# Kernel tuning notes

Measured on AMD Instinct MI355X. Metric: run time of the kernel, lower is better.

Reference implementation:

```python
import jax, jax.numpy as jnp
import numpy as np

CHEB_K = 3
HIDDEN = 64
HORIZON = 12
OUT_DIM = 1


def _supports(E, K):
    # adaptive adjacency: softmax(relu(E E^T)) rows, Chebyshev polynomial stack [K, N, N]
    A = jax.nn.softmax(jax.nn.relu(E @ E.T), axis=1)
    N = E.shape[0]
    s = [jnp.eye(N, dtype=E.dtype), A]
    for _ in range(2, K):
        s.append(2.0 * (A @ s[-1]) - s[-2])
    return jnp.stack(s, axis=0)


def _gconv(x, supports, W, b):
    # x: [B,N,C], supports: [K,N,N], W: [N,K,C,O], b: [N,O] -> [B,N,O]
    xg = jnp.einsum('knm,bmc->bnkc', supports, x)
    return jnp.einsum('bnkc,nkco->bno', xg, W) + b


def _agcrn_layer(x_seq, supports, gW, gb, uW, ub):
    # x_seq: [B,T,N,C]; returns full hidden sequence [B,T,N,H]
    B, T, N, _ = x_seq.shape
    h0 = jnp.zeros((B, N, HIDDEN), dtype=x_seq.dtype)

    def step(h, x):
        zr = jax.nn.sigmoid(_gconv(jnp.concatenate([x, h], axis=-1), supports, gW, gb))
        z, r = zr[..., :HIDDEN], zr[..., HIDDEN:]
        hc = jnp.tanh(_gconv(jnp.concatenate([x, z * h], axis=-1), supports, uW, ub))
        h_new = r * h + (1.0 - r) * hc
        return h_new, h_new

    _, hs = jax.lax.scan(step, h0, jnp.swapaxes(x_seq, 0, 1))  # [T,B,N,H]
    return jnp.swapaxes(hs, 0, 1)


def _forward(source, E, pools, conv_w, conv_b):
    supports = _supports(E, CHEB_K)
    cur = source
    for (gwp, gbp, uwp, ubp) in pools:
        # per-node weights from embedding pool (hoisted: E is constant over time)
        gW = jnp.einsum('nd,dkio->nkio', E, gwp)
        gb = E @ gbp
        uW = jnp.einsum('nd,dkio->nkio', E, uwp)
        ub = E @ ubp
        cur = _agcrn_layer(cur, supports, gW, gb, uW, ub)
    last = cur[:, -1]  # [B,N,H]
    # end_conv: Conv2d(1, horizon*out_dim, kernel=(1,H)) == linear over H per node
    y = jnp.einsum('bnh,oh->bon', last, conv_w) + conv_b[None, :, None]  # [B, horizon*out, N]
    B, _, N = y.shape
    y = y.reshape(B, HORIZON, OUT_DIM, N).transpose(0, 1, 3, 2)  # [B, horizon, N, out_dim]
    return y


def setup_inputs() -> dict:
    key = jax.random.key(0)
    ks = jax.random.split(key, 12)
    B, T, N, C, D, H = 64, 12, 2000, 1, 16, HIDDEN
    s = 0.1  # keep gates/tanh unsaturated
    return {
        'source': jax.random.normal(ks[0], (B, T, N, C), jnp.float32),
        'node_embeddings': jax.random.normal(ks[1], (N, D), jnp.float32),
        'gate_wpool_0': jax.random.normal(ks[2], (D, CHEB_K, C + H, 2 * H), jnp.float32) * s,
        'gate_bpool_0': jax.random.normal(ks[3], (D, 2 * H), jnp.float32) * s,
        'update_wpool_0': jax.random.normal(ks[4], (D, CHEB_K, C + H, H), jnp.float32) * s,
        'update_bpool_0': jax.random.normal(ks[5], (D, H), jnp.float32) * s,
        'gate_wpool_1': jax.random.normal(ks[6], (D, CHEB_K, 2 * H, 2 * H), jnp.float32) * s,
        'gate_bpool_1': jax.random.normal(ks[7], (D, 2 * H), jnp.float32) * s,
        'update_wpool_1': jax.random.normal(ks[8], (D, CHEB_K, 2 * H, H), jnp.float32) * s,
        'update_bpool_1': jax.random.normal(ks[9], (D, H), jnp.float32) * s,
        'conv_w': jax.random.normal(ks[10], (HORIZON * OUT_DIM, H), jnp.float32) * s,
        'conv_b': jax.random.normal(ks[11], (HORIZON * OUT_DIM,), jnp.float32) * s,
    }


def reference(source, node_embeddings, gate_wpool_0, gate_bpool_0, update_wpool_0,
              update_bpool_0, gate_wpool_1, gate_bpool_1, update_wpool_1,
              update_bpool_1, conv_w, conv_b):
    pools = [
        (gate_wpool_0, gate_bpool_0, update_wpool_0, update_bpool_0),
        (gate_wpool_1, gate_bpool_1, update_wpool_1, update_bpool_1),
    ]
    return _forward(source, node_embeddings, pools, conv_w, conv_b)
```

## Files before the change

### kernel.cpp

```cpp
#include <hip/hip_runtime.h>
#include <hip/hip_bf16.h>
#include <math.h>

#define NN 2000
#define DD 16
#define BB 64
#define TT 12
#define HH 64
#define MR 4000
#define SCL 2048.0f
#define ISCL (1.0f / 2048.0f)

typedef _Float16 f16;
typedef __attribute__((ext_vector_type(8))) _Float16 frag8h;
typedef __attribute__((ext_vector_type(4))) float floatx4;

__device__ inline float fin(float v) {
  return (v == v && v > -1e30f && v < 1e30f) ? v : 0.f;
}
__device__ inline float sigmoid_safe(float x) {
  float e = expf(-fabsf(x));
  float s = 1.f / (1.f + e);
  return x >= 0.f ? s : 1.f - s;
}
__device__ inline float tanh_safe(float x) {
  float e = expf(-2.f * fabsf(x));
  float r = (1.f - e) / (1.f + e);
  return x >= 0.f ? r : -r;
}
__device__ inline void split16(float v, f16& hi, f16& lo) {
  hi = (f16)v;
  lo = (f16)((v - (float)hi) * SCL);
}
__device__ inline void gll16(const void* g, void* l) {
  __builtin_amdgcn_global_load_lds((const __attribute__((address_space(1))) void*)g,
                                   (__attribute__((address_space(3))) void*)l, 16, 0, 0);
}

__global__ void kzero(float* p, int n) {
  int i = blockIdx.x * 256 + threadIdx.x;
  if (i < n) p[i] = 0.f;
}

__global__ __launch_bounds__(256) void ka(const float* __restrict__ E,
                                          float* __restrict__ A) {
  __shared__ float s[NN];
  __shared__ float red[256];
  int n = blockIdx.x;
  float en[DD];
#pragma unroll
  for (int d = 0; d < DD; ++d) en[d] = fin(E[n * DD + d]);
  float lmax = 0.f;
  for (int m = threadIdx.x; m < NN; m += 256) {
    float acc = 0.f;
#pragma unroll
    for (int d = 0; d < DD; ++d) acc += en[d] * fin(E[m * DD + d]);
    acc = fmaxf(acc, 0.f);
    s[m] = acc;
    lmax = fmaxf(lmax, acc);
  }
  red[threadIdx.x] = lmax;
  __syncthreads();
  for (int w = 128; w > 0; w >>= 1) {
    if (threadIdx.x < w) red[threadIdx.x] = fmaxf(red[threadIdx.x], red[threadIdx.x + w]);
    __syncthreads();
  }
  float mx = red[0];
  __syncthreads();
  float lsum = 0.f;
  for (int m = threadIdx.x; m < NN; m += 256) {
    float e = expf(s[m] - mx);
    s[m] = e;
    lsum += e;
  }
  red[threadIdx.x] = lsum;
  __syncthreads();
  for (int w = 128; w > 0; w >>= 1) {
    if (threadIdx.x < w) red[threadIdx.x] += red[threadIdx.x + w];
    __syncthreads();
  }
  float inv = 1.f / red[0];
  for (int m = threadIdx.x; m < NN; m += 256) A[(size_t)n * NN + m] = s[m] * inv;
}

#define TM 64
#define TK 32
__global__ __launch_bounds__(256) void kg(const float* __restrict__ A,
                                          const float* __restrict__ V,
                                          float* __restrict__ C, int cols) {
  __shared__ float As[TK][TM + 1];
  __shared__ float Bs[TK][TM + 1];
  int r0 = blockIdx.x * TM;
  int c0 = blockIdx.y * TM;
  int tid = threadIdx.x;
  int tx = tid % 16;
  int ty = tid / 16;
  float acc[4][4];
#pragma unroll
  for (int i = 0; i < 4; ++i)
#pragma unroll
    for (int j = 0; j < 4; ++j) acc[i][j] = 0.f;
  for (int k0 = 0; k0 < NN; k0 += TK) {
    for (int i = tid; i < TM * TK; i += 256) {
      int rr = i / TK, kk = i % TK;
      int gr = r0 + rr, gk = k0 + kk;
      As[kk][rr] = (gr < NN && gk < NN) ? A[(size_t)gr * NN + gk] : 0.f;
    }
    for (int i = tid; i < TK * TM; i += 256) {
      int kk = i / TM, cc = i % TM;
      int gk = k0 + kk, gc = c0 + cc;
      Bs[kk][cc] = (gk < NN && gc < cols) ? V[(size_t)gk * cols + gc] : 0.f;
    }
    __syncthreads();
#pragma unroll 4
    for (int kk = 0; kk < TK; ++kk) {
      float a[4], b[4];
#pragma unroll
      for (int i = 0; i < 4; ++i) a[i] = As[kk][ty * 4 + i];
#pragma unroll
      for (int j = 0; j < 4; ++j) b[j] = Bs[kk][tx * 4 + j];
#pragma unroll
      for (int i = 0; i < 4; ++i)
#pragma unroll
        for (int j = 0; j < 4; ++j) acc[i][j] += a[i] * b[j];
    }
    __syncthreads();
  }
#pragma unroll
  for (int i = 0; i < 4; ++i) {
    int gr = r0 + ty * 4 + i;
    if (gr >= NN) continue;
#pragma unroll
    for (int j = 0; j < 4; ++j) {
      int gc = c0 + tx * 4 + j;
      if (gc < cols) C[(size_t)gr * cols + gc] = acc[i][j];
    }
  }
}

__global__ void ksplitM(const float* __restrict__ A, const float* __restrict__ A2,
                        f16* __restrict__ Mh, f16* __restrict__ Ml) {
  int i = blockIdx.x * 256 + threadIdx.x;
  if (i >= MR * NN) return;
  int m = i / NN;
  int k = i % NN;
  float v;
  if (m < NN) v = A[(size_t)m * NN + k];
  else {
    int mm = m - NN;
    v = 2.f * A2[(size_t)mm * NN + k] - (mm == k ? 1.f : 0.f);
  }
  f16 hi, lo;
  split16(v, hi, lo);
  Mh[i] = hi;
  Ml[i] = lo;
}

__global__ __launch_bounds__(256) void kconvT(const float* __restrict__ V,
                                              f16* __restrict__ Th,
                                              f16* __restrict__ Tl, int cols) {
  __shared__ float sh[32][33];
  int k0 = blockIdx.x * 32;
  int c0 = blockIdx.y * 32;
  int tx = threadIdx.x % 32;
  int ty = threadIdx.x / 32;
#pragma unroll
  for (int i = 0; i < 4; ++i) {
    int r = k0 + ty + i * 8;
    int c = c0 + tx;
    sh[ty + i * 8][tx] = (r < NN && c < cols) ? V[(size_t)r * cols + c] : 0.f;
  }
  __syncthreads();
#pragma unroll
  for (int i = 0; i < 4; ++i) {
    int cc = c0 + ty + i * 8;
    int kk = k0 + tx;
    if (cc < cols && kk < NN) {
      f16 hi, lo;
      split16(sh[tx][ty + i * 8], hi, lo);
      Th[(size_t)cc * NN + kk] = hi;
      Tl[(size_t)cc * NN + kk] = lo;
    }
  }
}

#define KT 32
__global__ __launch_bounds__(256, 2) void kmm(const f16* __restrict__ Mh,
                                              const f16* __restrict__ Ml,
                                              const f16* __restrict__ Bh,
                                              const f16* __restrict__ Bl,
                                              float* __restrict__ C1,
                                              float* __restrict__ C2, int cols) {
  __shared__ __align__(16) f16 Ash[128 * KT];
  __shared__ __align__(16) f16 Asl[128 * KT];
  __shared__ __align__(16) f16 Bsh[128 * KT];
  __shared__ __align__(16) f16 Bsl[128 * KT];
  int tid = threadIdx.x;
  int lane = tid & 63;
  int wave = tid >> 6;
  int wr = wave >> 1;
  int wc = wave & 1;
  int bx = blockIdx.x;
  int by = blockIdx.y;
  floatx4 acc0[4][4], acc1[4][4];
#pragma unroll
  for (int i = 0; i < 4; ++i)
#pragma unroll
    for (int j = 0; j < 4; ++j) {
      acc0[i][j] = (floatx4){0.f, 0.f, 0.f, 0.f};
      acc1[i][j] = (floatx4){0.f, 0.f, 0.f, 0.f};
    }
  const frag8h zf = {0, 0, 0, 0, 0, 0, 0, 0};

  auto comp = [&]() {
    frag8h ah[4], al[4], bh[4], bl[4];
#pragma unroll
    for (int mi = 0; mi < 4; ++mi) {
      int jr = wr * 4 + mi;
      ah[mi] = *(const frag8h*)(&Ash[jr * 512 + lane * 8]);
      al[mi] = *(const frag8h*)(&Asl[jr * 512 + lane * 8]);
    }
#pragma unroll
    for (int ni = 0; ni < 4; ++ni) {
      int jc = wc * 4 + ni;
      bh[ni] = *(const frag8h*)(&Bsh[jc * 512 + lane * 8]);
      bl[ni] = *(const frag8h*)(&Bsl[jc * 512 + lane * 8]);
    }
#pragma unroll
    for (int mi = 0; mi < 4; ++mi)
#pragma unroll
      for (int ni = 0; ni < 4; ++ni) {
        acc0[mi][ni] = __builtin_amdgcn_mfma_f32_16x16x32_f16(ah[mi], bh[ni], acc0[mi][ni], 0, 0, 0);
        acc1[mi][ni] = __builtin_amdgcn_mfma_f32_16x16x32_f16(ah[mi], bl[ni], acc1[mi][ni], 0, 0, 0);
        acc1[mi][ni] = __builtin_amdgcn_mfma_f32_16x16x32_f16(al[mi], bh[ni], acc1[mi][ni], 0, 0, 0);
      }
  };

  const int lr = lane & 15;
  const int lq = lane >> 4;
  for (int k0 = 0; k0 + KT <= NN; k0 += KT) {
#pragma unroll
    for (int jj = 0; jj < 2; ++jj) {
      int j = wave * 2 + jj;
      int r = j * 16 + lr;
      size_t ko = (size_t)k0 + lq * 8;
      int gra = bx * 128 + r;
      if (gra < MR) {
        gll16(Mh + (size_t)gra * NN + ko, Ash + j * 512);
        gll16(Ml + (size_t)gra * NN + ko, Asl + j * 512);
      }
      int grb = by * 128 + r;
      if (grb < cols) {
        gll16(Bh + (size_t)grb * NN + ko, Bsh + j * 512);
        gll16(Bl + (size_t)grb * NN + ko, Bsl + j * 512);
      }
    }
    __syncthreads();
    comp();
    __syncthreads();
  }
  {
    int k0 = (NN / KT) * KT;
    if (k0 < NN) {
      for (int c = tid; c < 512; c += 256) {
        int j = c >> 6;
        int ll = c & 63;
        int q = ll >> 4;
        int rr = ll & 15;
        int r = j * 16 + rr;
        int gk = k0 + q * 8;
        bool kok = (gk + 8 <= NN);
        int gra = bx * 128 + r;
        bool aok = kok && (gra < MR);
        size_t ga = (size_t)gra * NN + gk;
        *(frag8h*)(&Ash[c * 8]) = aok ? *(const frag8h*)(Mh + ga) : zf;
        *(frag8h*)(&Asl[c * 8]) = aok ? *(const frag8h*)(Ml + ga) : zf;
        int grb = by * 128 + r;
        bool bok = kok && (grb < cols);
        size_t gb = (size_t)grb * NN + gk;
        *(frag8h*)(&Bsh[c * 8]) = bok ? *(const frag8h*)(Bh + gb) : zf;
        *(frag8h*)(&Bsl[c * 8]) = bok ? *(const frag8h*)(Bl + gb) : zf;
      }
      __syncthreads();
      comp();
      __syncthreads();
    }
  }
#pragma unroll
  for (int mi = 0; mi < 4; ++mi) {
#pragma unroll
    for (int ni = 0; ni < 4; ++ni) {
#pragma unroll
      for (int reg = 0; reg < 4; ++reg) {
        int row = bx * 128 + wr * 64 + mi * 16 + (lane >> 4) * 4 + reg;
        int col = by * 128 + wc * 64 + ni * 16 + (lane & 15);
        if (col >= cols || row >= MR) continue;
        float v = acc0[mi][ni][reg] + acc1[mi][ni][reg] * ISCL;
        if (row < NN) C1[(size_t)row * cols + col] = v;
        else C2[(size_t)(row - NN) * cols + col] = v;
      }
    }
  }
}

__global__ void kx(const float* __restrict__ src, float* __restrict__ xb,
                   int t, int b0, int CB) {
  int i = blockIdx.x * 256 + threadIdx.x;
  if (i >= NN * CB) return;
  int bb = i % CB;
  int n = i / CB;
  xb[i] = fin(src[((size_t)(b0 + bb) * TT + t) * NN + n]);
}

__global__ void kmulz(float* __restrict__ zb, const float* __restrict__ h, int n) {
  int i = blockIdx.x * 256 + threadIdx.x;
  if (i < n) zb[i] = zb[i] * h[i];
}

template <int O, int CB>
__global__ __launch_bounds__(256) void kgc(
    const float* __restrict__ x0, const float* __restrict__ x1, const float* __restrict__ x2,
    const float* __restrict__ wp, int Ctot, int base_c, int nC,
    const float* __restrict__ E, const float* __restrict__ bp,
    int act, int accum, float* outA, float* outB,
    int update, const float* __restrict__ rb, float* hio) {
  __shared__ float xs[8][CB + 1];
  __shared__ float ws[8][O];
  __shared__ float esm[DD];
  int n = blockIdx.x;
  int tid = threadIdx.x;
  int to = tid % 16;
  int tb = tid / 16;
  if (tid < DD) esm[tid] = fin(E[n * DD + tid]);
  __syncthreads();
  constexpr int NO = O / 16;
  constexpr int NB = CB / 16;
  float acc[NB][NO];
#pragma unroll
  for (int i = 0; i < NB; ++i)
#pragma unroll
    for (int j = 0; j < NO; ++j) acc[i][j] = 0.f;
  const size_t nb = (size_t)n * CB;
  for (int k = 0; k < 3; ++k) {
    const float* xk = (k == 0) ? x0 : (k == 1) ? x1 : x2;
    for (int c0 = 0; c0 < nC; c0 += 8) {
      int chunk = (nC - c0 < 8) ? (nC - c0) : 8;
      for (int i = tid; i < chunk * CB; i += 256) {
        int cc = i % chunk;
        int b = i / chunk;
        xs[cc][b] = xk[(nb + b) * nC + c0 + cc];
      }
      for (int i = tid; i < chunk * O; i += 256) {
        int o = i % O;
        int cc = i / O;
        int crow = base_c + c0 + cc;
        float wa = 0.f;
#pragma unroll
        for (int d = 0; d < DD; ++d)
          wa += esm[d] * fin(wp[((size_t)(d * 3 + k) * Ctot + crow) * O + o]);
        ws[cc][o] = wa;
      }
      __syncthreads();
      for (int cc = 0; cc < chunk; ++cc) {
        float xv[NB];
#pragma unroll
        for (int i = 0; i < NB; ++i) xv[i] = xs[cc][tb + 16 * i];
#pragma unroll
        for (int j = 0; j < NO; ++j) {
          float wv = ws[cc][to + 16 * j];
#pragma unroll
          for (int i = 0; i < NB; ++i) acc[i][j] += xv[i] * wv;
        }
      }
      __syncthreads();
    }
  }
#pragma unroll
  for (int i2 = 0; i2 < NB; ++i2) {
    int b = tb + 16 * i2;
#pragma unroll
    for (int j = 0; j < NO; ++j) {
      int o = to + 16 * j;
      float r = acc[i2][j];
      float* dst = (o < HH || !outB) ? (outA + (nb + b) * HH + (o % HH))
                                     : (outB + (nb + b) * HH + (o - HH));
      if (accum) r += *dst;
      if (bp) {
        float ba = 0.f;
#pragma unroll
        for (int d = 0; d < DD; ++d) ba += esm[d] * fin(bp[d * O + o]);
        r += ba;
      }
      r = fin(r);
      if (act == 1) r = sigmoid_safe(r);
      else if (act == 2) r = tanh_safe(r);
      if (update) {
        float rg = rb[(nb + b) * HH + o];
        float hold = hio[(nb + b) * HH + o];
        hio[(nb + b) * HH + o] = rg * hold + (1.f - rg) * r;
      } else {
        *dst = r;
      }
    }
  }
}

__global__ void kfin(const float* __restrict__ h1, const float* __restrict__ cw,
                     const float* __restrict__ cb, float* __restrict__ out,
                     int b0, int CB) {
  int idx = blockIdx.x * 256 + threadIdx.x;
  if (idx >= CB * TT * NN) return;
  int n = idx % NN;
  int o = (idx / NN) % TT;
  int bb = idx / (NN * TT);
  const float* hp = h1 + ((size_t)n * CB + bb) * HH;
  float acc = fin(cb[o]);
#pragma unroll
  for (int hh = 0; hh < HH; ++hh) acc += hp[hh] * fin(cw[o * HH + hh]);
  out[((size_t)(b0 + bb) * TT + o) * NN + n] = fin(acc);
}

template <int CB>
static void run_chunks(const float* src, const float* E,
                       const float* gwp0, const float* gbp0,
                       const float* uwp0, const float* ubp0,
                       const float* gwp1, const float* gbp1,
                       const float* uwp1, const float* ubp1,
                       const float* cw, const float* cb,
                       float* out, f16* Mh, f16* Ml,
                       char* wsp, size_t off0, hipStream_t stream) {
  size_t off = off0;
  auto allocf = [&](size_t nelem) {
    float* p = (float*)(wsp + off);
    off += (nelem * 4 + 255) & ~(size_t)255;
    return p;
  };
  auto alloch = [&](size_t nelem) {
    f16* p = (f16*)(wsp + off);
    off += (nelem * 2 + 255) & ~(size_t)255;
    return p;
  };
  const int C = CB * HH;
  const size_t NC = (size_t)NN * C;
  float* P1  = allocf(NC);
  float* P2  = allocf(NC);
  float* h0  = allocf(NC);
  float* h1  = allocf(NC);
  float* zb  = allocf(NC);
  float* rbf = allocf(NC);
  float* hc  = allocf(NC);
  f16* vh = alloch(NC);
  f16* vl = alloch(NC);
  float* xb0 = allocf((size_t)NN * CB);
  float* xb1 = allocf((size_t)NN * CB);
  float* xb2 = allocf((size_t)NN * CB);
  f16* xth = alloch((size_t)NN * CB);
  f16* xtl = alloch((size_t)NN * CB);

  const int EW = (int)((NC + 255) / 256);
  const int EWS = (NN * CB + 255) / 256;
  const dim3 gConv((NN + 31) / 32, (C + 31) / 32);
  const dim3 gConvX((NN + 31) / 32, (CB + 31) / 32);
  const dim3 gMM((MR + 127) / 128, (C + 127) / 128);
  const dim3 gMMX((MR + 127) / 128, (CB + 127) / 128);
  float* nul = nullptr;

  auto chain = [&](const float* V) {
    kconvT<<<gConv, 256, 0, stream>>>(V, vh, vl, C);
    kmm<<<gMM, 256, 0, stream>>>(Mh, Ml, vh, vl, P1, P2, C);
  };

  for (int b0 = 0; b0 < BB; b0 += CB) {
    kzero<<<EW, 256, 0, stream>>>(h0, (int)NC);
    kzero<<<EW, 256, 0, stream>>>(h1, (int)NC);
    for (int t = 0; t < TT; ++t) {
      kx<<<EWS, 256, 0, stream>>>(src, xb0, t, b0, CB);
      kconvT<<<gConvX, 256, 0, stream>>>(xb0, xth, xtl, CB);
      kmm<<<gMMX, 256, 0, stream>>>(Mh, Ml, xth, xtl, xb1, xb2, CB);
      chain(h0);
      kgc<128, CB><<<NN, 256, 0, stream>>>(h0, P1, P2, gwp0, 65, 1, 64, E, nullptr,
                                           0, 0, zb, rbf, 0, nul, nul);
      kgc<128, CB><<<NN, 256, 0, stream>>>(xb0, xb1, xb2, gwp0, 65, 0, 1, E, gbp0,
                                           1, 1, zb, rbf, 0, nul, nul);
      kgc<64, CB><<<NN, 256, 0, stream>>>(xb0, xb1, xb2, uwp0, 65, 0, 1, E, nullptr,
                                          0, 0, hc, nul, 0, nul, nul);
      kmulz<<<EW, 256, 0, stream>>>(zb, h0, (int)NC);
      chain(zb);
      kgc<64, CB><<<NN, 256, 0, stream>>>(zb, P1, P2, uwp0, 65, 1, 64, E, ubp0,
                                          2, 1, hc, nul, 1, rbf, h0);
      chain(h1);
      kgc<128, CB><<<NN, 256, 0, stream>>>(h1, P1, P2, gwp1, 128, 64, 64, E, nullptr,
                                           0, 0, zb, rbf, 0, nul, nul);
      chain(h0);
      kgc<128, CB><<<NN, 256, 0, stream>>>(h0, P1, P2, gwp1, 128, 0, 64, E, gbp1,
                                           1, 1, zb, rbf, 0, nul, nul);
      kgc<64, CB><<<NN, 256, 0, stream>>>(h0, P1, P2, uwp1, 128, 0, 64, E, nullptr,
                                          0, 0, hc, nul, 0, nul, nul);
      kmulz<<<EW, 256, 0, stream>>>(zb, h1, (int)NC);
      chain(zb);
      kgc<64, CB><<<NN, 256, 0, stream>>>(zb, P1, P2, uwp1, 128, 64, 64, E, ubp1,
                                          2, 1, hc, nul, 1, rbf, h1);
    }
    kfin<<<(CB * TT * NN + 255) / 256, 256, 0, stream>>>(h1, cw, cb, out, b0, CB);
  }
}

extern "C" void kernel_launch(void* const* d_in, const int* in_sizes, int n_in,
                              void* d_out, int out_size, void* d_ws, size_t ws_size,
                              hipStream_t stream) {
  const float* src  = (const float*)d_in[0];
  const float* E    = (const float*)d_in[1];
  const float* gwp0 = (const float*)d_in[2];
  const float* gbp0 = (const float*)d_in[3];
  const float* uwp0 = (const float*)d_in[4];
  const float* ubp0 = (const float*)d_in[5];
  const float* gwp1 = (const float*)d_in[6];
  const float* gbp1 = (const float*)d_in[7];
  const float* uwp1 = (const float*)d_in[8];
  const float* ubp1 = (const float*)d_in[9];
  const float* cw   = (const float*)d_in[10];
  const float* cb   = (const float*)d_in[11];
  float* out = (float*)d_out;
  (void)in_sizes; (void)n_in; (void)out_size;

  char* wsp = (char*)d_ws;
  size_t off = 0;
  f16* Mh = (f16*)(wsp + off); off += ((size_t)MR * NN * 2 + 255) & ~(size_t)255;
  f16* Ml = (f16*)(wsp + off); off += ((size_t)MR * NN * 2 + 255) & ~(size_t)255;
  size_t off0 = off;
  float* A  = (float*)(wsp + off0);
  float* A2 = (float*)(wsp + off0 + (((size_t)NN * NN * 4 + 255) & ~(size_t)255));

  ka<<<NN, 256, 0, stream>>>(E, A);
  {
    dim3 g((NN + TM - 1) / TM, (NN + TM - 1) / TM);
    kg<<<g, 256, 0, stream>>>(A, A, A2, NN);
  }
  ksplitM<<<(MR * NN + 255) / 256, 256, 0, stream>>>(A, A2, Mh, Ml);

  if (ws_size >= (size_t)320 * 1000 * 1000) {
    run_chunks<64>(src, E, gwp0, gbp0, uwp0, ubp0, gwp1, gbp1, uwp1, ubp1,
                   cw, cb, out, Mh, Ml, wsp, off0, stream);
  } else if (ws_size >= (size_t)185 * 1000 * 1000) {
    run_chunks<32>(src, E, gwp0, gbp0, uwp0, ubp0, gwp1, gbp1, uwp1, ubp1,
                   cw, cb, out, Mh, Ml, wsp, off0, stream);
  } else {
    run_chunks<16>(src, E, gwp0, gbp0, uwp0, ubp0, gwp1, gbp1, uwp1, ubp1,
                   cw, cb, out, Mh, Ml, wsp, off0, stream);
  }
}
```

Before: 61.85 ms.

## Batch input graph propagation over time, skip t=0 chains, reuse h0 propagation, swizzle XCDs

```diff
diff --git a/kernel.cpp b/kernel.cpp
--- a/kernel.cpp
+++ b/kernel.cpp
@@ -200,8 +200,14 @@
   int wave = tid >> 6;
   int wr = wave >> 1;
   int wc = wave & 1;
-  int bx = blockIdx.x;
-  int by = blockIdx.y;
+  int gx = gridDim.x;
+  int nwg = gx * gridDim.y;
+  int wg = blockIdx.y * gx + blockIdx.x;
+  int q = nwg >> 3, r = nwg & 7;
+  int xcd = wg & 7, lid = wg >> 3;
+  int swz = (xcd < r ? xcd * (q + 1) : r * (q + 1) + (xcd - r) * q) + lid;
+  int bx = swz % gx;
+  int by = swz / gx;
   floatx4 acc0[4][4], acc1[4][4];
 #pragma unroll
   for (int i = 0; i < 4; ++i)
@@ -242,14 +248,14 @@
 #pragma unroll
     for (int jj = 0; jj < 2; ++jj) {
       int j = wave * 2 + jj;
-      int r = j * 16 + lr;
+      int r2 = j * 16 + lr;
       size_t ko = (size_t)k0 + lq * 8;
-      int gra = bx * 128 + r;
+      int gra = bx * 128 + r2;
       if (gra < MR) {
         gll16(Mh + (size_t)gra * NN + ko, Ash + j * 512);
         gll16(Ml + (size_t)gra * NN + ko, Asl + j * 512);
       }
-      int grb = by * 128 + r;
+      int grb = by * 128 + r2;
       if (grb < cols) {
         gll16(Bh + (size_t)grb * NN + ko, Bsh + j * 512);
         gll16(Bl + (size_t)grb * NN + ko, Bsl + j * 512);
@@ -265,17 +271,17 @@
       for (int c = tid; c < 512; c += 256) {
         int j = c >> 6;
         int ll = c & 63;
-        int q = ll >> 4;
+        int qq = ll >> 4;
         int rr = ll & 15;
-        int r = j * 16 + rr;
-        int gk = k0 + q * 8;
+        int r2 = j * 16 + rr;
+        int gk = k0 + qq * 8;
         bool kok = (gk + 8 <= NN);
-        int gra = bx * 128 + r;
+        int gra = bx * 128 + r2;
         bool aok = kok && (gra < MR);
         size_t ga = (size_t)gra * NN + gk;
         *(frag8h*)(&Ash[c * 8]) = aok ? *(const frag8h*)(Mh + ga) : zf;
         *(frag8h*)(&Asl[c * 8]) = aok ? *(const frag8h*)(Ml + ga) : zf;
-        int grb = by * 128 + r;
+        int grb = by * 128 + r2;
         bool bok = kok && (grb < cols);
         size_t gb = (size_t)grb * NN + gk;
         *(frag8h*)(&Bsh[c * 8]) = bok ? *(const frag8h*)(Bh + gb) : zf;
@@ -312,6 +318,16 @@
   xb[i] = fin(src[((size_t)(b0 + bb) * TT + t) * NN + n]);
 }
 
+__global__ void kxa(const float* __restrict__ src, float* __restrict__ xa,
+                    int b0, int CB) {
+  int i = blockIdx.x * 256 + threadIdx.x;
+  if (i >= NN * TT * CB) return;
+  int bb = i % CB;
+  int t = (i / CB) % TT;
+  int n = i / (CB * TT);
+  xa[i] = fin(src[((size_t)(b0 + bb) * TT + t) * NN + n]);
+}
+
 __global__ void kmulz(float* __restrict__ zb, const float* __restrict__ h, int n) {
   int i = blockIdx.x * 256 + threadIdx.x;
   if (i < n) zb[i] = zb[i] * h[i];
@@ -320,7 +336,7 @@
 template <int O, int CB>
 __global__ __launch_bounds__(256) void kgc(
     const float* __restrict__ x0, const float* __restrict__ x1, const float* __restrict__ x2,
-    const float* __restrict__ wp, int Ctot, int base_c, int nC,
+    const float* __restrict__ wp, int Ctot, int base_c, int nC, int ldn,
     const float* __restrict__ E, const float* __restrict__ bp,
     int act, int accum, float* outA, float* outB,
     int update, const float* __restrict__ rb, float* hio) {
@@ -341,6 +357,7 @@
 #pragma unroll
     for (int j = 0; j < NO; ++j) acc[i][j] = 0.f;
   const size_t nb = (size_t)n * CB;
+  const size_t nx = (size_t)n * ldn;
   for (int k = 0; k < 3; ++k) {
     const float* xk = (k == 0) ? x0 : (k == 1) ? x1 : x2;
     for (int c0 = 0; c0 < nC; c0 += 8) {
@@ -348,7 +365,7 @@
       for (int i = tid; i < chunk * CB; i += 256) {
         int cc = i % chunk;
         int b = i / chunk;
-        xs[cc][b] = xk[(nb + b) * nC + c0 + cc];
+        xs[cc][b] = xk[nx + (size_t)b * nC + c0 + cc];
       }
       for (int i = tid; i < chunk * O; i += 256) {
         int o = i % O;
@@ -428,7 +445,7 @@
                        const float* uwp1, const float* ubp1,
                        const float* cw, const float* cb,
                        float* out, f16* Mh, f16* Ml,
-                       char* wsp, size_t off0, hipStream_t stream) {
+                       char* wsp, size_t off0, bool roomy, hipStream_t stream) {
   size_t off = off0;
   auto allocf = [&](size_t nelem) {
     float* p = (float*)(wsp + off);
@@ -441,6 +458,7 @@
     return p;
   };
   const int C = CB * HH;
+  const int XC = TT * CB;
   const size_t NC = (size_t)NN * C;
   float* P1  = allocf(NC);
   float* P2  = allocf(NC);
@@ -451,55 +469,107 @@
   float* hc  = allocf(NC);
   f16* vh = alloch(NC);
   f16* vl = alloch(NC);
-  float* xb0 = allocf((size_t)NN * CB);
-  float* xb1 = allocf((size_t)NN * CB);
-  float* xb2 = allocf((size_t)NN * CB);
-  f16* xth = alloch((size_t)NN * CB);
-  f16* xtl = alloch((size_t)NN * CB);
+  float *P1c = nullptr, *P2c = nullptr;
+  float *xa = nullptr, *xb1a = nullptr, *xb2a = nullptr;
+  float *xb0 = nullptr, *xb1 = nullptr, *xb2 = nullptr;
+  f16 *xth, *xtl;
+  if (roomy) {
+    P1c = allocf(NC);
+    P2c = allocf(NC);
+    xa   = allocf((size_t)NN * XC);
+    xb1a = allocf((size_t)NN * XC);
+    xb2a = allocf((size_t)NN * XC);
+    xth = alloch((size_t)NN * XC);
+    xtl = alloch((size_t)NN * XC);
+  } else {
+    xb0 = allocf((size_t)NN * CB);
+    xb1 = allocf((size_t)NN * CB);
+    xb2 = allocf((size_t)NN * CB);
+    xth = alloch((size_t)NN * CB);
+    xtl = alloch((size_t)NN * CB);
+  }
 
   const int EW = (int)((NC + 255) / 256);
-  const int EWS = (NN * CB + 255) / 256;
   const dim3 gConv((NN + 31) / 32, (C + 31) / 32);
-  const dim3 gConvX((NN + 31) / 32, (CB + 31) / 32);
   const dim3 gMM((MR + 127) / 128, (C + 127) / 128);
-  const dim3 gMMX((MR + 127) / 128, (CB + 127) / 128);
   float* nul = nullptr;
 
-  auto chain = [&](const float* V) {
+  auto chain_to = [&](const float* V, float* D1, float* D2) {
     kconvT<<<gConv, 256, 0, stream>>>(V, vh, vl, C);
-    kmm<<<gMM, 256, 0, stream>>>(Mh, Ml, vh, vl, P1, P2, C);
+    kmm<<<gMM, 256, 0, stream>>>(Mh, Ml, vh, vl, D1, D2, C);
   };
 
   for (int b0 = 0; b0 < BB; b0 += CB) {
     kzero<<<EW, 256, 0, stream>>>(h0, (int)NC);
     kzero<<<EW, 256, 0, stream>>>(h1, (int)NC);
+    if (roomy) {
+      kxa<<<((NN * XC) + 255) / 256, 256, 0, stream>>>(src, xa, b0, CB);
+      dim3 gcx((NN + 31) / 32, (XC + 31) / 32);
+      kconvT<<<gcx, 256, 0, stream>>>(xa, xth, xtl, XC);
+      dim3 gmx((MR + 127) / 128, (XC + 127) / 128);
+      kmm<<<gmx, 256, 0, stream>>>(Mh, Ml, xth, xtl, xb1a, xb2a, XC);
+    }
     for (int t = 0; t < TT; ++t) {
-      kx<<<EWS, 256, 0, stream>>>(src, xb0, t, b0, CB);
-      kconvT<<<gConvX, 256, 0, stream>>>(xb0, xth, xtl, CB);
-      kmm<<<gMMX, 256, 0, stream>>>(Mh, Ml, xth, xtl, xb1, xb2, CB);
-      chain(h0);
-      kgc<128, CB><<<NN, 256, 0, stream>>>(h0, P1, P2, gwp0, 65, 1, 64, E, nullptr,
+      const bool tz = (t == 0);
+      const float *xt0, *xt1, *xt2;
+      int xln;
+      if (roomy) {
+        xt0 = xa + t * CB;
+        xt1 = xb1a + t * CB;
+        xt2 = xb2a + t * CB;
+        xln = XC;
+      } else {
+        kx<<<(NN * CB + 255) / 256, 256, 0, stream>>>(src, xb0, t, b0, CB);
+        dim3 gcx((NN + 31) / 32, (CB + 31) / 32);
+        kconvT<<<gcx, 256, 0, stream>>>(xb0, xth, xtl, CB);
+        dim3 gmx((MR + 127) / 128, (CB + 127) / 128);
+        kmm<<<gmx, 256, 0, stream>>>(Mh, Ml, xth, xtl, xb1, xb2, CB);
+        xt0 = xb0; xt1 = xb1; xt2 = xb2;
+        xln = CB;
+      }
+      const float *g1, *g2;
+      if (tz) { g1 = h0; g2 = h0; }
+      else if (roomy) { g1 = P1c; g2 = P2c; }
+      else { chain_to(h0, P1, P2); g1 = P1; g2 = P2; }
+      kgc<128, CB><<<NN, 256, 0, stream>>>(h0, g1, g2, gwp0, 65, 1, 64, C, E, nullptr,
                                            0, 0, zb, rbf, 0, nul, nul);
-      kgc<128, CB><<<NN, 256, 0, stream>>>(xb0, xb1, xb2, gwp0, 65, 0, 1, E, gbp0,
+      kgc<128, CB><<<NN, 256, 0, stream>>>(xt0, xt1, xt2, gwp0, 65, 0, 1, xln, E, gbp0,
                                            1, 1, zb, rbf, 0, nul, nul);
-      kgc<64, CB><<<NN, 256, 0, stream>>>(xb0, xb1, xb2, uwp0, 65, 0, 1, E, nullptr,
+      kgc<64, CB><<<NN, 256, 0, stream>>>(xt0, xt1, xt2, uwp0, 65, 0, 1, xln, E, nullptr,
                                           0, 0, hc, nul, 0, nul, nul);
       kmulz<<<EW, 256, 0, stream>>>(zb, h0, (int)NC);
-      chain(zb);
-      kgc<64, CB><<<NN, 256, 0, stream>>>(zb, P1, P2, uwp0, 65, 1, 64, E, ubp0,
-                                          2, 1, hc, nul, 1, rbf, h0);
-      chain(h1);
-      kgc<128, CB><<<NN, 256, 0, stream>>>(h1, P1, P2, gwp1, 128, 64, 64, E, nullptr,
-                                           0, 0, zb, rbf, 0, nul, nul);
-      chain(h0);
-      kgc<128, CB><<<NN, 256, 0, stream>>>(h0, P1, P2, gwp1, 128, 0, 64, E, gbp1,
+      if (tz) {
+        kgc<64, CB><<<NN, 256, 0, stream>>>(zb, zb, zb, uwp0, 65, 1, 64, C, E, ubp0,
+                                            2, 1, hc, nul, 1, rbf, h0);
+      } else {
+        chain_to(zb, P1, P2);
+        kgc<64, CB><<<NN, 256, 0, stream>>>(zb, P1, P2, uwp0, 65, 1, 64, C, E, ubp0,
+                                            2, 1, hc, nul, 1, rbf, h0);
+      }
+      if (tz) {
+        kgc<128, CB><<<NN, 256, 0, stream>>>(h1, h1, h1, gwp1, 128, 64, 64, C, E, nullptr,
+                                             0, 0, zb, rbf, 0, nul, nul);
+      } else {
+        chain_to(h1, P1, P2);
+        kgc<128, CB><<<NN, 256, 0, stream>>>(h1, P1, P2, gwp1, 128, 64, 64, C, E, nullptr,
+                                             0, 0, zb, rbf, 0, nul, nul);
+      }
+      float* q1 = roomy ? P1c : P1;
+      float* q2 = roomy ? P2c : P2;
+      chain_to(h0, q1, q2);
+      kgc<128, CB><<<NN, 256, 0, stream>>>(h0, q1, q2, gwp1, 128, 0, 64, C, E, gbp1,
                                            1, 1, zb, rbf, 0, nul, nul);
-      kgc<64, CB><<<NN, 256, 0, stream>>>(h0, P1, P2, uwp1, 128, 0, 64, E, nullptr,
+      kgc<64, CB><<<NN, 256, 0, stream>>>(h0, q1, q2, uwp1, 128, 0, 64, C, E, nullptr,
                                           0, 0, hc, nul, 0, nul, nul);
       kmulz<<<EW, 256, 0, stream>>>(zb, h1, (int)NC);
-      chain(zb);
-      kgc<64, CB><<<NN, 256, 0, stream>>>(zb, P1, P2, uwp1, 128, 64, 64, E, ubp1,
-                                          2, 1, hc, nul, 1, rbf, h1);
+      if (tz) {
+        kgc<64, CB><<<NN, 256, 0, stream>>>(zb, zb, zb, uwp1, 128, 64, 64, C, E, ubp1,
+                                            2, 1, hc, nul, 1, rbf, h1);
+      } else {
+        chain_to(zb, P1, P2);
+        kgc<64, CB><<<NN, 256, 0, stream>>>(zb, P1, P2, uwp1, 128, 64, 64, C, E, ubp1,
+                                            2, 1, hc, nul, 1, rbf, h1);
+      }
     }
     kfin<<<(CB * TT * NN + 255) / 256, 256, 0, stream>>>(h1, cw, cb, out, b0, CB);
   }
@@ -538,14 +608,23 @@
   }
   ksplitM<<<(MR * NN + 255) / 256, 256, 0, stream>>>(A, A2, Mh, Ml);
 
-  if (ws_size >= (size_t)320 * 1000 * 1000) {
+  if (ws_size >= (size_t)400 * 1000 * 1000) {
     run_chunks<64>(src, E, gwp0, gbp0, uwp0, ubp0, gwp1, gbp1, uwp1, ubp1,
-                   cw, cb, out, Mh, Ml, wsp, off0, stream);
+                   cw, cb, out, Mh, Ml, wsp, off0, true, stream);
+  } else if (ws_size >= (size_t)320 * 1000 * 1000) {
+    run_chunks<64>(src, E, gwp0, gbp0, uwp0, ubp0, gwp1, gbp1, uwp1, ubp1,
+                   cw, cb, out, Mh, Ml, wsp, off0, false, stream);
+  } else if (ws_size >= (size_t)225 * 1000 * 1000) {
+    run_chunks<32>(src, E, gwp0, gbp0, uwp0, ubp0, gwp1, gbp1, uwp1, ubp1,
+                   cw, cb, out, Mh, Ml, wsp, off0, true, stream);
   } else if (ws_size >= (size_t)185 * 1000 * 1000) {
     run_chunks<32>(src, E, gwp0, gbp0, uwp0, ubp0, gwp1, gbp1, uwp1, ubp1,
-                   cw, cb, out, Mh, Ml, wsp, off0, stream);
+                   cw, cb, out, Mh, Ml, wsp, off0, false, stream);
+  } else if (ws_size >= (size_t)130 * 1000 * 1000) {
+    run_chunks<16>(src, E, gwp0, gbp0, uwp0, ubp0, gwp1, gbp1, uwp1, ubp1,
+                   cw, cb, out, Mh, Ml, wsp, off0, true, stream);
   } else {
     run_chunks<16>(src, E, gwp0, gbp0, uwp0, ubp0, gwp1, gbp1, uwp1, ubp1,
-                   cw, cb, out, Mh, Ml, wsp, off0, stream);
-  }
-}
+                   cw, cb, out, Mh, Ml, wsp, off0, false, stream);
+  }
+}
```

Measured after the change: 54.50 ms. 1.13x faster.
